# Performance work log

Measured on AMD Instinct MI355X. Metric: run time of the kernel, lower is better.

## Reference

```python
import jax, jax.numpy as jnp
import numpy as np

P_MASK = 0.2
HALF = (2, 25, 25)            # n_consecutive // 2 for (T, H, W)
NPIX = 5 * 51 * 51            # np.prod(n_consecutive) = 13005


def setup_inputs() -> dict:
    key = jax.random.key(0)
    ks = jax.random.split(key, 10)
    B, T, H, W, C = 4, 32, 224, 224, 3
    N = 2000
    frames = jax.random.normal(ks[0], (B, T, H, W, C), dtype=jnp.float32)
    mask_token = jax.random.normal(ks[1], (C,), dtype=jnp.float32)
    b = jax.random.randint(ks[2], (N,), 0, B)
    t = jax.random.randint(ks[3], (N,), 0, T)
    h = jax.random.randint(ks[4], (N,), 0, H)
    w = jax.random.randint(ks[5], (N,), 0, W)
    rb = jax.random.randint(ks[6], (1,), 0, B)
    rt = jax.random.randint(ks[7], (1,), 0, T)
    rh = jax.random.randint(ks[8], (1,), 0, H)
    rw = jax.random.randint(ks[9], (1,), 0, W)
    return dict(frames=frames, mask_token=mask_token, b=b, t=t, h=h, w=w,
                rb=rb, rt=rt, rh=rh, rw=rw)


def _axis_mask(idx, half, size):
    # [n_box, size] float indicator of max(0, idx-half) <= pos < min(idx+half, size-1)
    lo = jnp.maximum(idx - half, 0)[:, None]
    hi = jnp.minimum(idx + half, size - 1)[:, None]   # torch slice upper bound uses size-1
    pos = jnp.arange(size)[None, :]
    return ((pos >= lo) & (pos < hi)).astype(jnp.float32)


def _box_union(b, t, h, w, B, T, H, W):
    # union of all boxes as a single rank-1-factor contraction (no per-box scatter)
    bi = (jnp.arange(B)[None, :] == b[:, None]).astype(jnp.float32)
    ti = _axis_mask(t, HALF[0], T)
    hi = _axis_mask(h, HALF[1], H)
    wi = _axis_mask(w, HALF[2], W)
    return jnp.einsum('ib,it,ih,iw->bthw', bi, ti, hi, wi) > 0


def reference(frames, mask_token, b, t, h, w, rb, rt, rh, rw):
    B, T, H, W, C = frames.shape
    tnpix = B * T * H * W
    n1 = int(tnpix * P_MASK * 0.8 // NPIX)
    n2 = int(tnpix * P_MASK * 0.1 // NPIX)
    R1 = _box_union(b[:n1], t[:n1], h[:n1], w[:n1], B, T, H, W)
    R2 = _box_union(b[n1:n1 + n2], t[n1:n1 + n2], h[n1:n1 + n2], w[n1:n1 + n2], B, T, H, W)
    R3 = _box_union(b[n1 + n2:n1 + 2 * n2], t[n1 + n2:n1 + 2 * n2],
                    h[n1 + n2:n1 + 2 * n2], w[n1 + n2:n1 + 2 * n2], B, T, H, W)
    random_token = frames[rb[0], rt[0], rh[0], rw[0]]   # [C]
    out = jnp.where(R1[..., None], mask_token, frames)
    out = jnp.where(R2[..., None], random_token, out)
    M = (R1 | R2 | R3).reshape(B, T, -1).any(axis=-1)
    return out, M
```

## Files before the change

kernel.cpp:

```cpp
#include <hip/hip_runtime.h>

namespace {
constexpr int B_ = 4, T_ = 32, H_ = 224, W_ = 224;
constexpr int HW_ = H_ * W_;
constexpr int NPIX_ = B_ * T_ * HW_;
constexpr int N1_ = 79;
constexpr int N2_ = 9;
constexpr int NBOX_RW_ = N1_ + N2_;
constexpr int NBOX_M_  = N1_ + 2 * N2_;
constexpr int HALF_T = 2, HALF_HW = 25;
constexpr int GPT_ = 16;
constexpr int GPR_ = W_ / GPT_;
constexpr int GPS_ = H_ * GPR_;
constexpr int NGRP_ = B_ * T_ * GPS_;
constexpr int F4_TOTAL_ = NPIX_ * 3 / 4;
constexpr int ABLK_ = F4_TOTAL_ / 256;
}

typedef float floatx4 __attribute__((ext_vector_type(4)));

__global__ __launch_bounds__(256) void build_masks(
    const float* __restrict__ frames,
    const int* __restrict__ bb, const int* __restrict__ tt,
    const int* __restrict__ hh, const int* __restrict__ ww,
    const int* __restrict__ rb, const int* __restrict__ rt,
    const int* __restrict__ rh, const int* __restrict__ rw,
    unsigned* __restrict__ gmask, float* __restrict__ rtok,
    float* __restrict__ Mout)
{
    __shared__ int4 r1[NBOX_RW_];
    __shared__ int4 r2[N2_];
    __shared__ int c1, c2, c3;
    const int s = blockIdx.x;
    const int tid = threadIdx.x;
    if (tid == 0) { c1 = 0; c2 = 0; c3 = 0; }
    __syncthreads();

    if (s == 0 && tid == 0) {
        long idx = (((long)rb[0] * T_ + rt[0]) * H_ + rh[0]) * W_ + rw[0];
        rtok[0] = frames[idx * 3 + 0];
        rtok[1] = frames[idx * 3 + 1];
        rtok[2] = frames[idx * 3 + 2];
    }

    const int sb = s / T_, st = s % T_;
    if (tid < NBOX_M_) {
        const int i = tid;
        int tlo = max(tt[i] - HALF_T, 0);
        int thi = min(tt[i] + HALF_T, T_ - 1);
        if (bb[i] == sb && st >= tlo && st < thi) {
            if (i >= NBOX_RW_) {
                atomicAdd(&c3, 1);
            } else {
                int4 r;
                r.x = max(hh[i] - HALF_HW, 0);
                r.y = min(hh[i] + HALF_HW, H_ - 1);
                r.z = max(ww[i] - HALF_HW, 0);
                r.w = min(ww[i] + HALF_HW, W_ - 1);
                if (i < N1_) r1[atomicAdd(&c1, 1)] = r;
                else         r2[atomicAdd(&c2, 1)] = r;
            }
        }
    }
    __syncthreads();

    if (tid == 0) Mout[s] = (c1 + c2 + c3) > 0 ? 1.0f : 0.0f;

    const int n1 = c1, n2 = c2;
    for (int g = tid; g < GPS_; g += 256) {
        int h  = g / GPR_;
        int w0 = (g - h * GPR_) * GPT_;
        unsigned m1 = 0, m2 = 0;
        for (int j = 0; j < n1; ++j) {
            int4 r = r1[j];
            if (h >= r.x && h < r.y) {
                int lo = max(r.z - w0, 0), hi = min(r.w - w0, GPT_);
                if (hi > lo) m1 |= ((1u << (hi - lo)) - 1u) << lo;
            }
        }
        for (int j = 0; j < n2; ++j) {
            int4 r = r2[j];
            if (h >= r.x && h < r.y) {
                int lo = max(r.z - w0, 0), hi = min(r.w - w0, GPT_);
                if (hi > lo) m2 |= ((1u << (hi - lo)) - 1u) << lo;
            }
        }
        gmask[s * GPS_ + g] = m1 | (m2 << 16);
    }
}

__global__ __launch_bounds__(256) void apply_mask(
    const floatx4* __restrict__ frames4, const float* __restrict__ mtok,
    const unsigned* __restrict__ gmask, const float* __restrict__ rtok,
    floatx4* __restrict__ out4)
{
    const unsigned g4 = blockIdx.x * 256u + threadIdx.x;
    const unsigned q  = __umulhi(g4, 0xAAAAAAABu) >> 1;
    const unsigned ph = g4 - 3u * q;
    const unsigned m  = (4u * g4 - ph) * 0xAAAAAAABu;
    const unsigned w0i = m >> 4;
    const unsigned wa = gmask[w0i];
    const unsigned wb = gmask[(m + 1u) >> 4];

    floatx4 v = __builtin_nontemporal_load(&frames4[g4]);

    if (wa | wb) {
        float m0 = mtok[0], m1 = mtok[1], m2 = mtok[2];
        float r0 = rtok[0], r1 = rtok[1], r2 = rtok[2];
        float a0 = ph == 0 ? m0 : (ph == 1 ? m1 : m2);
        float a1 = ph == 0 ? m1 : (ph == 1 ? m2 : m0);
        float a2 = ph == 0 ? m2 : (ph == 1 ? m0 : m1);
        float b0 = ph == 0 ? r0 : (ph == 1 ? r1 : r2);
        float b1 = ph == 0 ? r1 : (ph == 1 ? r2 : r0);
        float b2 = ph == 0 ? r2 : (ph == 1 ? r0 : r1);
        const unsigned d1 = (ph + 1) / 3, d2 = (ph + 2) / 3;
        unsigned p1 = m + d1, p2 = m + d2, p3 = m + 1u;
        unsigned w1 = ((p1 >> 4) == w0i) ? wa : wb;
        unsigned w2 = ((p2 >> 4) == w0i) ? wa : wb;
        unsigned w3 = ((p3 >> 4) == w0i) ? wa : wb;
        unsigned q0 = m & 15u, q1 = p1 & 15u, q2 = p2 & 15u, q3 = p3 & 15u;
        v.x = ((wa >> (q0 + 16)) & 1u) ? b0 : (((wa >> q0) & 1u) ? a0 : v.x);
        v.y = ((w1 >> (q1 + 16)) & 1u) ? b1 : (((w1 >> q1) & 1u) ? a1 : v.y);
        v.z = ((w2 >> (q2 + 16)) & 1u) ? b2 : (((w2 >> q2) & 1u) ? a2 : v.z);
        v.w = ((w3 >> (q3 + 16)) & 1u) ? b0 : (((w3 >> q3) & 1u) ? a0 : v.w);
    }

    __builtin_nontemporal_store(v, &out4[g4]);
}

extern "C" void kernel_launch(void* const* d_in, const int* in_sizes, int n_in,
                              void* d_out, int out_size, void* d_ws, size_t ws_size,
                              hipStream_t stream)
{
    const float* frames = (const float*)d_in[0];
    const float* mtok   = (const float*)d_in[1];
    const int* b  = (const int*)d_in[2];
    const int* t  = (const int*)d_in[3];
    const int* h  = (const int*)d_in[4];
    const int* w  = (const int*)d_in[5];
    const int* rb = (const int*)d_in[6];
    const int* rt = (const int*)d_in[7];
    const int* rh = (const int*)d_in[8];
    const int* rw = (const int*)d_in[9];

    unsigned* gmask = (unsigned*)d_ws;
    float*    rtok  = (float*)((char*)d_ws + (size_t)NGRP_ * 4);

    float* out_frames = (float*)d_out;
    float* out_M      = out_frames + (long)NPIX_ * 3;

    build_masks<<<B_ * T_, 256, 0, stream>>>(frames, b, t, h, w, rb, rt, rh, rw,
                                             gmask, rtok, out_M);

    apply_mask<<<ABLK_, 256, 0, stream>>>((const floatx4*)frames, mtok, gmask,
                                          rtok, (floatx4*)out_frames);
}
```

Baseline: 162.4 us.

## Fuse mask construction into apply kernel with per-block box culling

Merges the two kernels into a single pass. Each 256-thread block works out its own slice and row range, gathers the boxes that overlap those rows into shared memory, and tests each pixel directly against them. This removes the second launch, the global bitmask write and read, and the serial dependency between the kernels. In exchange, every block re-reads the box index arrays and runs a per-pixel loop over the boxes it kept. The code relies on each slice spanning exactly 147 blocks.

```diff
diff --git a/kernel.cpp b/kernel.cpp
--- a/kernel.cpp
+++ b/kernel.cpp
@@ -9,120 +9,108 @@
 constexpr int NBOX_RW_ = N1_ + N2_;
 constexpr int NBOX_M_  = N1_ + 2 * N2_;
 constexpr int HALF_T = 2, HALF_HW = 25;
-constexpr int GPT_ = 16;
-constexpr int GPR_ = W_ / GPT_;
-constexpr int GPS_ = H_ * GPR_;
-constexpr int NGRP_ = B_ * T_ * GPS_;
 constexpr int F4_TOTAL_ = NPIX_ * 3 / 4;
 constexpr int ABLK_ = F4_TOTAL_ / 256;
+constexpr int BPS_ = 147;
 }
 
 typedef float floatx4 __attribute__((ext_vector_type(4)));
 
-__global__ __launch_bounds__(256) void build_masks(
-    const float* __restrict__ frames,
+__global__ __launch_bounds__(256) void fused_mask(
+    const floatx4* __restrict__ frames4, const float* __restrict__ frames,
+    const float* __restrict__ mtok,
     const int* __restrict__ bb, const int* __restrict__ tt,
     const int* __restrict__ hh, const int* __restrict__ ww,
     const int* __restrict__ rb, const int* __restrict__ rt,
     const int* __restrict__ rh, const int* __restrict__ rw,
-    unsigned* __restrict__ gmask, float* __restrict__ rtok,
-    float* __restrict__ Mout)
+    floatx4* __restrict__ out4, float* __restrict__ Mout)
 {
-    __shared__ int4 r1[NBOX_RW_];
-    __shared__ int4 r2[N2_];
-    __shared__ int c1, c2, c3;
-    const int s = blockIdx.x;
     const int tid = threadIdx.x;
-    if (tid == 0) { c1 = 0; c2 = 0; c3 = 0; }
+    const unsigned g4 = blockIdx.x * 256u + tid;
+
+    floatx4 v = __builtin_nontemporal_load(&frames4[g4]);
+
+    const int s  = blockIdx.x / BPS_;
+    const int lb = blockIdx.x - s * BPS_;
+    const int sb = s / T_, st = s - sb * T_;
+
+    __shared__ int4 R1s[NBOX_RW_];
+    __shared__ int4 R2s[N2_];
+    __shared__ int c1, c2, cM;
+    __shared__ float tok[6];
+
+    if (tid == 0) { c1 = 0; c2 = 0; cM = 0; }
     __syncthreads();
 
-    if (s == 0 && tid == 0) {
-        long idx = (((long)rb[0] * T_ + rt[0]) * H_ + rh[0]) * W_ + rw[0];
-        rtok[0] = frames[idx * 3 + 0];
-        rtok[1] = frames[idx * 3 + 1];
-        rtok[2] = frames[idx * 3 + 2];
-    }
-
-    const int sb = s / T_, st = s % T_;
     if (tid < NBOX_M_) {
         const int i = tid;
         int tlo = max(tt[i] - HALF_T, 0);
         int thi = min(tt[i] + HALF_T, T_ - 1);
         if (bb[i] == sb && st >= tlo && st < thi) {
-            if (i >= NBOX_RW_) {
-                atomicAdd(&c3, 1);
-            } else {
+            cM = 1;
+            if (i < NBOX_RW_) {
+                const int pf = (int)((1024u * blockIdx.x) / 3u) - s * HW_;
+                const int pl = (int)((1024u * blockIdx.x + 1023u) / 3u) - s * HW_;
+                const int hlo_blk = pf / W_, hhi_blk = pl / W_;
                 int4 r;
                 r.x = max(hh[i] - HALF_HW, 0);
                 r.y = min(hh[i] + HALF_HW, H_ - 1);
                 r.z = max(ww[i] - HALF_HW, 0);
                 r.w = min(ww[i] + HALF_HW, W_ - 1);
-                if (i < N1_) r1[atomicAdd(&c1, 1)] = r;
-                else         r2[atomicAdd(&c2, 1)] = r;
+                if (r.x <= hhi_blk && r.y > hlo_blk) {
+                    if (i < N1_) R1s[atomicAdd(&c1, 1)] = r;
+                    else         R2s[atomicAdd(&c2, 1)] = r;
+                }
             }
         }
+    } else if (tid == 128) {
+        tok[0] = mtok[0]; tok[1] = mtok[1]; tok[2] = mtok[2];
+        long idx = (((long)rb[0] * T_ + rt[0]) * H_ + rh[0]) * W_ + rw[0];
+        tok[3] = frames[idx * 3 + 0];
+        tok[4] = frames[idx * 3 + 1];
+        tok[5] = frames[idx * 3 + 2];
     }
     __syncthreads();
 
-    if (tid == 0) Mout[s] = (c1 + c2 + c3) > 0 ? 1.0f : 0.0f;
+    if (lb == 0 && tid == 0) Mout[s] = cM ? 1.0f : 0.0f;
 
     const int n1 = c1, n2 = c2;
-    for (int g = tid; g < GPS_; g += 256) {
-        int h  = g / GPR_;
-        int w0 = (g - h * GPR_) * GPT_;
-        unsigned m1 = 0, m2 = 0;
+    if (n1 | n2) {
+        const unsigned q  = __umulhi(g4, 0xAAAAAAABu) >> 1;
+        const unsigned ph = g4 - 3u * q;
+        const unsigned m  = (4u * g4 - ph) * 0xAAAAAAABu;
+        const int lpA = (int)m - s * HW_;
+        const int hA = lpA / W_, wA = lpA - hA * W_;
+        const int lpB = lpA + 1;
+        const int hB = lpB / W_, wB = lpB - hB * W_;
+        int in1a = 0, in1b = 0, in2a = 0, in2b = 0;
         for (int j = 0; j < n1; ++j) {
-            int4 r = r1[j];
-            if (h >= r.x && h < r.y) {
-                int lo = max(r.z - w0, 0), hi = min(r.w - w0, GPT_);
-                if (hi > lo) m1 |= ((1u << (hi - lo)) - 1u) << lo;
-            }
+            int4 r = R1s[j];
+            in1a |= (hA >= r.x) & (hA < r.y) & (wA >= r.z) & (wA < r.w);
+            in1b |= (hB >= r.x) & (hB < r.y) & (wB >= r.z) & (wB < r.w);
         }
         for (int j = 0; j < n2; ++j) {
-            int4 r = r2[j];
-            if (h >= r.x && h < r.y) {
-                int lo = max(r.z - w0, 0), hi = min(r.w - w0, GPT_);
-                if (hi > lo) m2 |= ((1u << (hi - lo)) - 1u) << lo;
-            }
+            int4 r = R2s[j];
+            in2a |= (hA >= r.x) & (hA < r.y) & (wA >= r.z) & (wA < r.w);
+            in2b |= (hB >= r.x) & (hB < r.y) & (wB >= r.z) & (wB < r.w);
         }
-        gmask[s * GPS_ + g] = m1 | (m2 << 16);
-    }
-}
-
-__global__ __launch_bounds__(256) void apply_mask(
-    const floatx4* __restrict__ frames4, const float* __restrict__ mtok,
-    const unsigned* __restrict__ gmask, const float* __restrict__ rtok,
-    floatx4* __restrict__ out4)
-{
-    const unsigned g4 = blockIdx.x * 256u + threadIdx.x;
-    const unsigned q  = __umulhi(g4, 0xAAAAAAABu) >> 1;
-    const unsigned ph = g4 - 3u * q;
-    const unsigned m  = (4u * g4 - ph) * 0xAAAAAAABu;
-    const unsigned w0i = m >> 4;
-    const unsigned wa = gmask[w0i];
-    const unsigned wb = gmask[(m + 1u) >> 4];
-
-    floatx4 v = __builtin_nontemporal_load(&frames4[g4]);
-
-    if (wa | wb) {
-        float m0 = mtok[0], m1 = mtok[1], m2 = mtok[2];
-        float r0 = rtok[0], r1 = rtok[1], r2 = rtok[2];
-        float a0 = ph == 0 ? m0 : (ph == 1 ? m1 : m2);
-        float a1 = ph == 0 ? m1 : (ph == 1 ? m2 : m0);
-        float a2 = ph == 0 ? m2 : (ph == 1 ? m0 : m1);
-        float b0 = ph == 0 ? r0 : (ph == 1 ? r1 : r2);
-        float b1 = ph == 0 ? r1 : (ph == 1 ? r2 : r0);
-        float b2 = ph == 0 ? r2 : (ph == 1 ? r0 : r1);
-        const unsigned d1 = (ph + 1) / 3, d2 = (ph + 2) / 3;
-        unsigned p1 = m + d1, p2 = m + d2, p3 = m + 1u;
-        unsigned w1 = ((p1 >> 4) == w0i) ? wa : wb;
-        unsigned w2 = ((p2 >> 4) == w0i) ? wa : wb;
-        unsigned w3 = ((p3 >> 4) == w0i) ? wa : wb;
-        unsigned q0 = m & 15u, q1 = p1 & 15u, q2 = p2 & 15u, q3 = p3 & 15u;
-        v.x = ((wa >> (q0 + 16)) & 1u) ? b0 : (((wa >> q0) & 1u) ? a0 : v.x);
-        v.y = ((w1 >> (q1 + 16)) & 1u) ? b1 : (((w1 >> q1) & 1u) ? a1 : v.y);
-        v.z = ((w2 >> (q2 + 16)) & 1u) ? b2 : (((w2 >> q2) & 1u) ? a2 : v.z);
-        v.w = ((w3 >> (q3 + 16)) & 1u) ? b0 : (((w3 >> q3) & 1u) ? a0 : v.w);
+        if (in1a | in1b | in2a | in2b) {
+            float m0 = tok[0], m1 = tok[1], m2 = tok[2];
+            float r0 = tok[3], r1 = tok[4], r2 = tok[5];
+            float a0 = ph == 0 ? m0 : (ph == 1 ? m1 : m2);
+            float a1 = ph == 0 ? m1 : (ph == 1 ? m2 : m0);
+            float a2 = ph == 0 ? m2 : (ph == 1 ? m0 : m1);
+            float b0 = ph == 0 ? r0 : (ph == 1 ? r1 : r2);
+            float b1 = ph == 0 ? r1 : (ph == 1 ? r2 : r0);
+            float b2 = ph == 0 ? r2 : (ph == 1 ? r0 : r1);
+            const unsigned d1 = (ph + 1) / 3, d2 = (ph + 2) / 3;
+            int i1y = d1 ? in1b : in1a, i2y = d1 ? in2b : in2a;
+            int i1z = d2 ? in1b : in1a, i2z = d2 ? in2b : in2a;
+            v.x = in2a ? b0 : (in1a ? a0 : v.x);
+            v.y = i2y  ? b1 : (i1y  ? a1 : v.y);
+            v.z = i2z  ? b2 : (i1z  ? a2 : v.z);
+            v.w = in2b ? b0 : (in1b ? a0 : v.w);
+        }
     }
 
     __builtin_nontemporal_store(v, &out4[g4]);
@@ -143,15 +131,10 @@
     const int* rh = (const int*)d_in[8];
     const int* rw = (const int*)d_in[9];
 
-    unsigned* gmask = (unsigned*)d_ws;
-    float*    rtok  = (float*)((char*)d_ws + (size_t)NGRP_ * 4);
-
     float* out_frames = (float*)d_out;
     float* out_M      = out_frames + (long)NPIX_ * 3;
 
-    build_masks<<<B_ * T_, 256, 0, stream>>>(frames, b, t, h, w, rb, rt, rh, rw,
-                                             gmask, rtok, out_M);
-
-    apply_mask<<<ABLK_, 256, 0, stream>>>((const floatx4*)frames, mtok, gmask,
-                                          rtok, (floatx4*)out_frames);
+    fused_mask<<<ABLK_, 256, 0, stream>>>((const floatx4*)frames, frames, mtok,
+                                          b, t, h, w, rb, rt, rh, rw,
+                                          (floatx4*)out_frames, out_M);
 }
```

Result: faster. 154.3 us (-5.0%).
